# Kernel tuning notes

Measured on AMD Instinct MI355X. Metric: run time of the kernel, lower is better.

The kernel has to match this reference:

```python
import jax, jax.numpy as jnp
import numpy as np

M, N, K, C, G = 16384, 131072, 16, 128, 8
EPS_BN = 1e-5


def _bn(x, g, b):
    # inference-mode BatchNorm1d (running_mean=0, running_var=1)
    return x * (g / jnp.sqrt(1.0 + EPS_BN)) + b


def setup_inputs() -> dict:
    key = jax.random.key(0)
    ks = jax.random.split(key, 16)
    f32 = jnp.float32
    s = 0.05
    return {
        "query_feat": jax.random.normal(ks[0], (M, C), f32),
        "context_feat": jax.random.normal(ks[1], (N, C), f32),
        "query_coord": jax.random.normal(ks[2], (M, 3), f32),
        "context_coord": jax.random.normal(ks[3], (N, 3), f32),
        "Wq": jax.random.normal(ks[4], (C, C), f32) * s,
        "bq": jnp.zeros((C,), f32),
        "gq": jnp.ones((C,), f32),
        "betaq": jnp.zeros((C,), f32),
        "Wk": jax.random.normal(ks[5], (C, C), f32) * s,
        "bk": jnp.zeros((C,), f32),
        "gk": jnp.ones((C,), f32),
        "betak": jnp.zeros((C,), f32),
        "Wv": jax.random.normal(ks[6], (C, C), f32) * s,
        "bv": jnp.zeros((C,), f32),
        "Wp1": jax.random.normal(ks[7], (3, C), f32) * s,
        "bp1": jnp.zeros((C,), f32),
        "gp1": jnp.ones((C,), f32),
        "betap1": jnp.zeros((C,), f32),
        "Wp2": jax.random.normal(ks[8], (C, C), f32) * s,
        "bp2": jnp.zeros((C,), f32),
        "Ww1": jax.random.normal(ks[9], (C, G), f32) * s,
        "bw1": jnp.zeros((G,), f32),
        "gw1": jnp.ones((G,), f32),
        "betaw1": jnp.zeros((G,), f32),
        "Ww2": jax.random.normal(ks[10], (G, G), f32) * s,
        "bw2": jnp.zeros((G,), f32),
        "knn_indexes": jax.random.randint(ks[11], (M, K), 0, N, dtype=jnp.int32),
    }


def reference(query_feat, context_feat, query_coord, context_coord,
              Wq, bq, gq, betaq, Wk, bk, gk, betak, Wv, bv,
              Wp1, bp1, gp1, betap1, Wp2, bp2,
              Ww1, bw1, gw1, betaw1, Ww2, bw2, knn_indexes):
    q = jax.nn.relu(_bn(query_feat @ Wq + bq, gq, betaq))              # (M, C)
    k = jax.nn.relu(_bn(context_feat @ Wk + bk, gk, betak))            # (N, C)
    v = context_feat @ Wv + bv                                         # (N, C)

    mask = knn_indexes >= 0                                            # (M, K); -1 = padded neighbor
    idx = jnp.where(mask, knn_indexes, 0)
    mf = mask[..., None].astype(q.dtype)                               # (M, K, 1)

    key_g = k[idx] * mf                                                # (M, K, C) gather (zero row for -1)
    val_g = v[idx] * mf                                                # (M, K, C)
    pos = (context_coord[idx] - query_coord[:, None, :]) * mf          # (M, K, 3) relative position

    # positional-encoding bias branch (pe_bias=True, pe_multiplier=False)
    peb = jax.nn.relu(_bn(pos @ Wp1 + bp1, gp1, betap1)) @ Wp2 + bp2   # (M, K, C)
    rel = key_g - q[:, None, :] + peb                                  # (M, K, C)
    val_g = val_g + peb

    # grouped vector attention weights
    w = jax.nn.relu(_bn(rel @ Ww1 + bw1, gw1, betaw1)) @ Ww2 + bw2     # (M, K, G)
    w = jax.nn.softmax(w, axis=1) * mf                                 # softmax over neighbors, mask padded

    m_, k_ = idx.shape
    c_ = q.shape[-1]
    g_ = w.shape[-1]
    out = jnp.einsum('mkgi,mkg->mgi', val_g.reshape(m_, k_, g_, c_ // g_), w)
    return out.reshape(m_, c_)
```

## Files before the change

### kernel.cpp

```cpp
#include <hip/hip_runtime.h>

#define C 128
#define G 8
#define KNN 16
#define QB 4
#define EPS 1e-5f

typedef unsigned short u16;
typedef __attribute__((ext_vector_type(8))) short short8;
typedef __attribute__((ext_vector_type(4))) float float4v;

union frag_u { short8 v; u16 u[8]; };

__device__ inline u16 f2bf(float f) {
    unsigned u = __builtin_bit_cast(unsigned, f);
    unsigned r = (u + 0x7fffu + ((u >> 16) & 1u)) >> 16;
    return (u16)r;
}
__device__ inline float bf2f(u16 h) {
    unsigned u = ((unsigned)h) << 16;
    return __builtin_bit_cast(float, u);
}

__global__ __launch_bounds__(256) void prep_w(
    const float* __restrict__ Wk, const float* __restrict__ Wv,
    const float* __restrict__ Wq, const float* __restrict__ Wp2,
    const float* __restrict__ Ww1, u16* __restrict__ dst)
{
    const int b = blockIdx.x, t = threadIdx.x;
    if (b < 16) {
        const int mi = b >> 2, qt = b & 3;
        const float* W = mi == 0 ? Wk : mi == 1 ? Wv : mi == 2 ? Wq : Wp2;
        u16* d = dst + mi * 16384;
        for (int e = qt * 4096 + t; e < (qt + 1) * 4096; e += 256) {
            const int k = e >> 7, n = e & 127;
            const int cb = n >> 4, lan = n & 15;
            const int kk = k >> 5, quad = (k >> 3) & 3, j = k & 7;
            d[(((cb * 4 + kk) * 4 + quad) * 16 + lan) * 8 + j] = f2bf(W[e]);
        }
    } else {
        u16* d = dst + 4 * 16384;
        for (int e = t; e < 4096; e += 256) {
            const int j = e & 7, lan = (e >> 3) & 15;
            const int quad = (e >> 7) & 3, kk = e >> 9;
            const int k = kk * 32 + quad * 8 + j;
            d[e] = lan < 8 ? f2bf(Ww1[k * G + lan]) : (u16)0;
        }
    }
}

__global__ __launch_bounds__(256) void proj_all(
    const float* __restrict__ Xc, const float* __restrict__ Xq,
    const u16* __restrict__ PWk, const float* __restrict__ bk,
    const float* __restrict__ gk, const float* __restrict__ betak,
    const u16* __restrict__ PWv, const float* __restrict__ bv,
    const u16* __restrict__ PWq, const float* __restrict__ bq,
    const float* __restrict__ gq, const float* __restrict__ betaq,
    u16* __restrict__ kout, u16* __restrict__ vout, u16* __restrict__ qout,
    int nkv)
{
    __shared__ u16 Xs[64 * 136];
    const int t = threadIdx.x;
    const int w = t >> 6, l = t & 63;
    const int quad = l >> 4, lan = l & 15;
    const bool isq = (int)blockIdx.x >= nkv;
    const long long row0 = (long long)(isq ? blockIdx.x - nkv : blockIdx.x) * 64;
    const float* X = isq ? Xq : Xc;

    {
        const float4* Xv = (const float4*)(X + row0 * C);
#pragma unroll
        for (int i = 0; i < 8; i++) {
            const int e = t + 256 * i;
            const int r = e >> 5, c4 = e & 31;
            const float4 f = Xv[e];
            uint2 p;
            p.x = (unsigned)f2bf(f.x) | ((unsigned)f2bf(f.y) << 16);
            p.y = (unsigned)f2bf(f.z) | ((unsigned)f2bf(f.w) << 16);
            *(uint2*)(&Xs[r * 136 + c4 * 4]) = p;
        }
    }
    __syncthreads();

    if (!isq) {
        unsigned vp[2][4][2];
        {
            short8 Bf[2][4];
#pragma unroll
            for (int ct = 0; ct < 2; ct++) {
                const int cb = w * 2 + ct;
#pragma unroll
                for (int kk = 0; kk < 4; kk++)
                    Bf[ct][kk] = *(const short8*)(PWv + (((cb * 4 + kk) * 4 + quad) * 16 + lan) * 8);
            }
            float4v acc[2][4];
#pragma unroll
            for (int ct = 0; ct < 2; ct++)
#pragma unroll
                for (int rt = 0; rt < 4; rt++) acc[ct][rt] = (float4v)0.f;
#pragma unroll
            for (int rt = 0; rt < 4; rt++)
#pragma unroll
                for (int kk = 0; kk < 4; kk++) {
                    const short8 A = *(const short8*)(&Xs[(rt * 16 + lan) * 136 + kk * 32 + quad * 8]);
#pragma unroll
                    for (int ct = 0; ct < 2; ct++)
                        acc[ct][rt] = __builtin_amdgcn_mfma_f32_16x16x32_bf16(
                            A, Bf[ct][kk], acc[ct][rt], 0, 0, 0);
                }
#pragma unroll
            for (int ct = 0; ct < 2; ct++) {
                const float bb = bv[w * 32 + ct * 16 + lan];
#pragma unroll
                for (int rt = 0; rt < 4; rt++)
#pragma unroll
                    for (int h = 0; h < 2; h++)
                        vp[ct][rt][h] = (unsigned)f2bf(acc[ct][rt][2 * h] + bb)
                                      | ((unsigned)f2bf(acc[ct][rt][2 * h + 1] + bb) << 16);
            }
        }
        float4v acck[2][4];
        {
            short8 Bf[2][4];
#pragma unroll
            for (int ct = 0; ct < 2; ct++) {
                const int cb = w * 2 + ct;
#pragma unroll
                for (int kk = 0; kk < 4; kk++)
                    Bf[ct][kk] = *(const short8*)(PWk + (((cb * 4 + kk) * 4 + quad) * 16 + lan) * 8);
            }
#pragma unroll
            for (int ct = 0; ct < 2; ct++)
#pragma unroll
                for (int rt = 0; rt < 4; rt++) acck[ct][rt] = (float4v)0.f;
#pragma unroll
            for (int rt = 0; rt < 4; rt++)
#pragma unroll
                for (int kk = 0; kk < 4; kk++) {
                    const short8 A = *(const short8*)(&Xs[(rt * 16 + lan) * 136 + kk * 32 + quad * 8]);
#pragma unroll
                    for (int ct = 0; ct < 2; ct++)
                        acck[ct][rt] = __builtin_amdgcn_mfma_f32_16x16x32_bf16(
                            A, Bf[ct][kk], acck[ct][rt], 0, 0, 0);
                }
        }
        __syncthreads();

#pragma unroll
        for (int ct = 0; ct < 2; ct++) {
            const int cg = w * 32 + ct * 16 + lan;
            const float bb = bk[cg];
            const float sc = gk[cg] * rsqrtf(1.f + EPS);
            const float sh = betak[cg];
#pragma unroll
            for (int rt = 0; rt < 4; rt++)
#pragma unroll
                for (int reg = 0; reg < 4; reg++) {
                    float y = (acck[ct][rt][reg] + bb) * sc + sh;
                    y = y > 0.f ? y : 0.f;
                    Xs[(rt * 16 + quad * 4 + reg) * 136 + cg] = f2bf(y);
                }
        }
        __syncthreads();
#pragma unroll
        for (int i = 0; i < 4; i++) {
            const int e = t + 256 * i;
            const int r = e >> 4, cc = (e & 15) * 8;
            *(short8*)(kout + (row0 + r) * C + cc) = *(const short8*)(&Xs[r * 136 + cc]);
        }
        __syncthreads();

#pragma unroll
        for (int ct = 0; ct < 2; ct++) {
            const int cg = w * 32 + ct * 16 + lan;
#pragma unroll
            for (int rt = 0; rt < 4; rt++)
#pragma unroll
                for (int h = 0; h < 2; h++) {
                    Xs[(rt * 16 + quad * 4 + 2 * h) * 136 + cg]     = (u16)(vp[ct][rt][h] & 0xffffu);
                    Xs[(rt * 16 + quad * 4 + 2 * h + 1) * 136 + cg] = (u16)(vp[ct][rt][h] >> 16);
                }
        }
        __syncthreads();
#pragma unroll
        for (int i = 0; i < 4; i++) {
            const int e = t + 256 * i;
            const int r = e >> 4, cc = (e & 15) * 8;
            *(short8*)(vout + (row0 + r) * C + cc) = *(const short8*)(&Xs[r * 136 + cc]);
        }
    } else {
        short8 Bf[2][4];
#pragma unroll
        for (int ct = 0; ct < 2; ct++) {
            const int cb = w * 2 + ct;
#pragma unroll
            for (int kk = 0; kk < 4; kk++)
                Bf[ct][kk] = *(const short8*)(PWq + (((cb * 4 + kk) * 4 + quad) * 16 + lan) * 8);
        }
        float4v acc[2][4];
#pragma unroll
        for (int ct = 0; ct < 2; ct++)
#pragma unroll
            for (int rt = 0; rt < 4; rt++) acc[ct][rt] = (float4v)0.f;
#pragma unroll
        for (int rt = 0; rt < 4; rt++)
#pragma unroll
            for (int kk = 0; kk < 4; kk++) {
                const short8 A = *(const short8*)(&Xs[(rt * 16 + lan) * 136 + kk * 32 + quad * 8]);
#pragma unroll
                for (int ct = 0; ct < 2; ct++)
                    acc[ct][rt] = __builtin_amdgcn_mfma_f32_16x16x32_bf16(
                        A, Bf[ct][kk], acc[ct][rt], 0, 0, 0);
            }
        __syncthreads();
#pragma unroll
        for (int ct = 0; ct < 2; ct++) {
            const int cg = w * 32 + ct * 16 + lan;
            const float bb = bq[cg];
            const float sc = gq[cg] * rsqrtf(1.f + EPS);
            const float sh = betaq[cg];
#pragma unroll
            for (int rt = 0; rt < 4; rt++)
#pragma unroll
                for (int reg = 0; reg < 4; reg++) {
                    float y = (acc[ct][rt][reg] + bb) * sc + sh;
                    y = y > 0.f ? y : 0.f;
                    Xs[(rt * 16 + quad * 4 + reg) * 136 + cg] = f2bf(y);
                }
        }
        __syncthreads();
#pragma unroll
        for (int i = 0; i < 4; i++) {
            const int e = t + 256 * i;
            const int r = e >> 4, cc = (e & 15) * 8;
            *(short8*)(qout + (row0 + r) * C + cc) = *(const short8*)(&Xs[r * 136 + cc]);
        }
    }
}

__global__ __launch_bounds__(256) void attn5(
    const u16* __restrict__ qbuf, const u16* __restrict__ kbuf,
    const u16* __restrict__ vbuf,
    const float* __restrict__ qcoord, const float* __restrict__ ccoord,
    const float* __restrict__ Wp1, const float* __restrict__ bp1,
    const float* __restrict__ gp1, const float* __restrict__ betap1,
    const u16* __restrict__ PWp2, const float* __restrict__ bp2,
    const u16* __restrict__ PWw1, const float* __restrict__ bw1,
    const float* __restrict__ gw1, const float* __restrict__ betaw1,
    const float* __restrict__ Ww2, const float* __restrict__ bw2,
    const int* __restrict__ knn, float* __restrict__ out)
{
    __shared__ u16   fA[64 * 136];
    __shared__ float pxs[64], pys[64], pzs[64];
    __shared__ int   idxs[64];
    __shared__ float wl[QB * 16 * G];

    const int t = threadIdx.x;
    const int w = t >> 6, l = t & 63;
    const int quad = l >> 4, lan = l & 15;
    const int m0 = blockIdx.x * QB;
    const int rsub = t >> 4;
    const int c8 = (t & 15) * 8;

    if (t < 64) {
        const int q = t >> 4;
        const int ii = knn[(m0 + q) * KNN + (t & 15)];
        const float mf = ii >= 0 ? 1.f : 0.f;
        const int i0 = ii >= 0 ? ii : 0;
        idxs[t] = ii;
        pxs[t] = (ccoord[i0 * 3 + 0] - qcoord[(m0 + q) * 3 + 0]) * mf;
        pys[t] = (ccoord[i0 * 3 + 1] - qcoord[(m0 + q) * 3 + 1]) * mf;
        pzs[t] = (ccoord[i0 * 3 + 2] - qcoord[(m0 + q) * 3 + 2]) * mf;
    }
    __syncthreads();

    {
        const int c = t & 127, hh = t >> 7;
        const float w0 = Wp1[c], w1_ = Wp1[C + c], w2_ = Wp1[2 * C + c];
        const float sc = gp1[c] * rsqrtf(1.f + EPS);
        const float bb = bp1[c], sh = betap1[c];
#pragma unroll
        for (int r2 = 0; r2 < 32; r2++) {
            const int r = hh * 32 + r2;
            float y = fmaf(pxs[r], w0, fmaf(pys[r], w1_, fmaf(pzs[r], w2_, bb)));
            y = y * sc + sh;
            y = y > 0.f ? y : 0.f;
            fA[r * 136 + c] = f2bf(y);
        }
    }
    __syncthreads();

    float4v acc[2][4];
    {
        short8 Bf[2][4];
#pragma unroll
        for (int ct = 0; ct < 2; ct++) {
            const int cb = w * 2 + ct;
#pragma unroll
            for (int kk = 0; kk < 4; kk++)
                Bf[ct][kk] = *(const short8*)(PWp2 + (((cb * 4 + kk) * 4 + quad) * 16 + lan) * 8);
        }
#pragma unroll
        for (int ct = 0; ct < 2; ct++)
#pragma unroll
            for (int q = 0; q < 4; q++) acc[ct][q] = (float4v)0.f;
#pragma unroll
        for (int q = 0; q < 4; q++)
#pragma unroll
            for (int kk = 0; kk < 4; kk++) {
                const short8 A = *(const short8*)(&fA[(q * 16 + lan) * 136 + kk * 32 + quad * 8]);
#pragma unroll
                for (int ct = 0; ct < 2; ct++)
                    acc[ct][q] = __builtin_amdgcn_mfma_f32_16x16x32_bf16(
                        A, Bf[ct][kk], acc[ct][q], 0, 0, 0);
            }
    }
    __syncthreads();

    {
        const float bb0 = bp2[w * 32 + lan];
        const float bb1 = bp2[w * 32 + 16 + lan];
#pragma unroll
        for (int ct = 0; ct < 2; ct++)
#pragma unroll
            for (int q = 0; q < 4; q++)
#pragma unroll
                for (int reg = 0; reg < 4; reg++)
                    fA[(q * 16 + quad * 4 + reg) * 136 + w * 32 + ct * 16 + lan] =
                        f2bf(acc[ct][q][reg] + (ct ? bb1 : bb0));
    }
    __syncthreads();

    short8 valr[4];
    {
#pragma unroll
        for (int p = 0; p < 4; p++) {
            const int r = p * 16 + rsub;
            const int ii = idxs[r];
            const float mf = ii >= 0 ? 1.f : 0.f;
            const size_t i0 = ii >= 0 ? ii : 0;
            frag_u kgv, vgv, qgv, peb, relv, valv;
            kgv.v = *(const short8*)(kbuf + i0 * C + c8);
            vgv.v = *(const short8*)(vbuf + i0 * C + c8);
            qgv.v = *(const short8*)(qbuf + (size_t)(m0 + p) * C + c8);
            peb.v = *(const short8*)(&fA[r * 136 + c8]);
#pragma unroll
            for (int j = 0; j < 8; j++) {
                const float pe = bf2f(peb.u[j]);
                relv.u[j] = f2bf(fmaf(bf2f(kgv.u[j]), mf, pe - bf2f(qgv.u[j])));
                valv.u[j] = f2bf(fmaf(bf2f(vgv.u[j]), mf, pe));
            }
            *(short8*)(&fA[r * 136 + c8]) = relv.v;
            valr[p] = valv.v;
        }
    }
    __syncthreads();

    {
        short8 Bw[4];
#pragma unroll
        for (int kk = 0; kk < 4; kk++)
            Bw[kk] = *(const short8*)(PWw1 + ((kk * 4 + quad) * 16 + lan) * 8);
        float4v a4 = (float4v)0.f;
#pragma unroll
        for (int kk = 0; kk < 4; kk++) {
            const short8 A = *(const short8*)(&fA[(w * 16 + lan) * 136 + kk * 32 + quad * 8]);
            a4 = __builtin_amdgcn_mfma_f32_16x16x32_bf16(A, Bw[kk], a4, 0, 0, 0);
        }
        if (lan < G) {
            const int g = lan;
            const float sc = gw1[g] * rsqrtf(1.f + EPS);
            const float bb = bw1[g], sh = betaw1[g];
#pragma unroll
            for (int reg = 0; reg < 4; reg++) {
                const int j = quad * 4 + reg;
                float y = (a4[reg] + bb) * sc + sh;
                wl[w * 128 + j * 8 + g] = y > 0.f ? y : 0.f;
            }
        }
    }
    __syncthreads();

#pragma unroll
    for (int p = 0; p < 4; p++)
        *(short8*)(&fA[(p * 16 + rsub) * 136 + c8]) = valr[p];

    if (t < QB * G) {
        const int q = t >> 3, g2 = t & 7;
        float w2c[G];
#pragma unroll
        for (int g = 0; g < G; g++) w2c[g] = Ww2[g * G + g2];
        const float bb = bw2[g2];
        float lg[KNN], mx = -1e30f;
#pragma unroll
        for (int j = 0; j < KNN; j++) {
            float a = bb;
#pragma unroll
            for (int g = 0; g < G; g++) a = fmaf(wl[q * 128 + j * 8 + g], w2c[g], a);
            lg[j] = a;
            mx = fmaxf(mx, a);
        }
        float sum = 0.f;
#pragma unroll
        for (int j = 0; j < KNN; j++) { lg[j] = __expf(lg[j] - mx); sum += lg[j]; }
        const float inv = 1.f / sum;
#pragma unroll
        for (int j = 0; j < KNN; j++) {
            const float mf = idxs[q * 16 + j] >= 0 ? 1.f : 0.f;
            wl[q * 128 + j * 8 + g2] = lg[j] * inv * mf;
        }
    }
    __syncthreads();

#pragma unroll
    for (int i = 0; i < 2; i++) {
        const int e = t + 256 * i;
        const int q = e >> 7, c = e & 127, g = c >> 4;
        float a = 0.f;
#pragma unroll
        for (int j = 0; j < KNN; j++)
            a = fmaf(bf2f(fA[(q * 16 + j) * 136 + c]), wl[q * 128 + j * 8 + g], a);
        out[(size_t)(m0 + q) * C + c] = a;
    }
}

extern "C" void kernel_launch(void* const* d_in, const int* in_sizes, int n_in,
                              void* d_out, int out_size, void* d_ws, size_t ws_size,
                              hipStream_t stream)
{
    const float* query_feat    = (const float*)d_in[0];
    const float* context_feat  = (const float*)d_in[1];
    const float* query_coord   = (const float*)d_in[2];
    const float* context_coord = (const float*)d_in[3];
    const float* Wq    = (const float*)d_in[4];
    const float* bq    = (const float*)d_in[5];
    const float* gq    = (const float*)d_in[6];
    const float* betaq = (const float*)d_in[7];
    const float* Wk    = (const float*)d_in[8];
    const float* bk    = (const float*)d_in[9];
    const float* gk    = (const float*)d_in[10];
    const float* betak = (const float*)d_in[11];
    const float* Wv    = (const float*)d_in[12];
    const float* bv    = (const float*)d_in[13];
    const float* Wp1   = (const float*)d_in[14];
    const float* bp1   = (const float*)d_in[15];
    const float* gp1   = (const float*)d_in[16];
    const float* betap1= (const float*)d_in[17];
    const float* Wp2   = (const float*)d_in[18];
    const float* bp2   = (const float*)d_in[19];
    const float* Ww1   = (const float*)d_in[20];
    const float* bw1   = (const float*)d_in[21];
    const float* gw1   = (const float*)d_in[22];
    const float* betaw1= (const float*)d_in[23];
    const float* Ww2   = (const float*)d_in[24];
    const float* bw2   = (const float*)d_in[25];
    const int*   knn   = (const int*)d_in[26];

    const int M = in_sizes[0] / C;
    const int N = in_sizes[1] / C;

    u16* kb = (u16*)d_ws;
    u16* vb = kb + (size_t)N * C;
    u16* qb = vb + (size_t)N * C;
    u16* pw = qb + (size_t)M * C;
    u16* pWk  = pw;
    u16* pWv  = pw + 16384;
    u16* pWq  = pw + 2 * 16384;
    u16* pWp2 = pw + 3 * 16384;
    u16* pWw1 = pw + 4 * 16384;

    prep_w<<<17, 256, 0, stream>>>(Wk, Wv, Wq, Wp2, Ww1, pw);
    proj_all<<<N / 64 + M / 64, 256, 0, stream>>>(
        context_feat, query_feat,
        pWk, bk, gk, betak, pWv, bv,
        pWq, bq, gq, betaq,
        kb, vb, qb, N / 64);
    attn5<<<M / QB, 256, 0, stream>>>(qb, kb, vb, query_coord, context_coord,
                                      Wp1, bp1, gp1, betap1, pWp2, bp2,
                                      pWw1, bw1, gw1, betaw1, Ww2, bw2,
                                      knn, (float*)d_out);
}
```

Before: 225.5 us.

## Fold Ww1 projection into K/Q/PE precompute to shrink gathered key data

Uses linearity of rel @ Ww1 = k@Ww1 - q@Ww1 + peb@Ww1 to project k and q down to 8 groups inside the projection kernel, storing K and Q as N×8 and M×8 instead of full 128-wide rows. Wp2@Ww1 and bp2@Ww1 are precomputed so the attention kernel gets the PE contribution from one extra MFMA. This removes the 128-channel key and query gathers and their full-width writes, and the value gather is now issued at kernel start to overlap with the PE work. The cost is extra MFMA work in the projection kernel and different bf16 rounding points, since the products are rounded to bf16 at 8 channels.

```diff
diff --git a/kernel.cpp b/kernel.cpp
--- a/kernel.cpp
+++ b/kernel.cpp
@@ -25,7 +25,8 @@
 __global__ __launch_bounds__(256) void prep_w(
     const float* __restrict__ Wk, const float* __restrict__ Wv,
     const float* __restrict__ Wq, const float* __restrict__ Wp2,
-    const float* __restrict__ Ww1, u16* __restrict__ dst)
+    const float* __restrict__ Ww1, const float* __restrict__ bp2,
+    u16* __restrict__ dst, float* __restrict__ cw1)
 {
     const int b = blockIdx.x, t = threadIdx.x;
     if (b < 16) {
@@ -38,13 +39,31 @@
             const int kk = k >> 5, quad = (k >> 3) & 3, j = k & 7;
             d[(((cb * 4 + kk) * 4 + quad) * 16 + lan) * 8 + j] = f2bf(W[e]);
         }
-    } else {
+    } else if (b == 16) {
         u16* d = dst + 4 * 16384;
         for (int e = t; e < 4096; e += 256) {
             const int j = e & 7, lan = (e >> 3) & 15;
             const int quad = (e >> 7) & 3, kk = e >> 9;
             const int k = kk * 32 + quad * 8 + j;
             d[e] = lan < 8 ? f2bf(Ww1[k * G + lan]) : (u16)0;
+        }
+    } else {
+        u16* d = dst + 4 * 16384 + 4096;
+        for (int e = t; e < 4096; e += 256) d[e] = 0;
+        __syncthreads();
+#pragma unroll
+        for (int it = 0; it < 4; it++) {
+            const int k = it * 32 + (t >> 3), g = t & 7;
+            float a = 0.f;
+            for (int i = 0; i < C; i++)
+                a = fmaf(Wp2[k * C + i], Ww1[i * G + g], a);
+            const int kk = k >> 5, quad = (k >> 3) & 3, j = k & 7;
+            d[((kk * 4 + quad) * 16 + g) * 8 + j] = f2bf(a);
+        }
+        if (t < G) {
+            float a = 0.f;
+            for (int i = 0; i < C; i++) a = fmaf(bp2[i], Ww1[i * G + t], a);
+            cw1[t] = a;
         }
     }
 }
@@ -56,7 +75,8 @@
     const u16* __restrict__ PWv, const float* __restrict__ bv,
     const u16* __restrict__ PWq, const float* __restrict__ bq,
     const float* __restrict__ gq, const float* __restrict__ betaq,
-    u16* __restrict__ kout, u16* __restrict__ vout, u16* __restrict__ qout,
+    const u16* __restrict__ PWw1b,
+    u16* __restrict__ vout, u16* __restrict__ Kp, u16* __restrict__ Qp,
     int nkv)
 {
     __shared__ u16 Xs[64 * 136];
@@ -162,11 +182,23 @@
                 }
         }
         __syncthreads();
-#pragma unroll
-        for (int i = 0; i < 4; i++) {
-            const int e = t + 256 * i;
-            const int r = e >> 4, cc = (e & 15) * 8;
-            *(short8*)(kout + (row0 + r) * C + cc) = *(const short8*)(&Xs[r * 136 + cc]);
+
+        {
+            short8 Bw[4];
+#pragma unroll
+            for (int kk = 0; kk < 4; kk++)
+                Bw[kk] = *(const short8*)(PWw1b + ((kk * 4 + quad) * 16 + lan) * 8);
+            float4v ka = (float4v)0.f;
+#pragma unroll
+            for (int kk = 0; kk < 4; kk++) {
+                const short8 A = *(const short8*)(&Xs[(w * 16 + lan) * 136 + kk * 32 + quad * 8]);
+                ka = __builtin_amdgcn_mfma_f32_16x16x32_bf16(A, Bw[kk], ka, 0, 0, 0);
+            }
+            if (lan < G) {
+#pragma unroll
+                for (int reg = 0; reg < 4; reg++)
+                    Kp[(row0 + w * 16 + quad * 4 + reg) * G + lan] = f2bf(ka[reg]);
+            }
         }
         __syncthreads();
 
@@ -189,29 +221,31 @@
             *(short8*)(vout + (row0 + r) * C + cc) = *(const short8*)(&Xs[r * 136 + cc]);
         }
     } else {
-        short8 Bf[2][4];
-#pragma unroll
-        for (int ct = 0; ct < 2; ct++) {
-            const int cb = w * 2 + ct;
-#pragma unroll
-            for (int kk = 0; kk < 4; kk++)
-                Bf[ct][kk] = *(const short8*)(PWq + (((cb * 4 + kk) * 4 + quad) * 16 + lan) * 8);
-        }
         float4v acc[2][4];
-#pragma unroll
-        for (int ct = 0; ct < 2; ct++)
-#pragma unroll
-            for (int rt = 0; rt < 4; rt++) acc[ct][rt] = (float4v)0.f;
-#pragma unroll
-        for (int rt = 0; rt < 4; rt++)
-#pragma unroll
-            for (int kk = 0; kk < 4; kk++) {
-                const short8 A = *(const short8*)(&Xs[(rt * 16 + lan) * 136 + kk * 32 + quad * 8]);
-#pragma unroll
-                for (int ct = 0; ct < 2; ct++)
-                    acc[ct][rt] = __builtin_amdgcn_mfma_f32_16x16x32_bf16(
-                        A, Bf[ct][kk], acc[ct][rt], 0, 0, 0);
-            }
+        {
+            short8 Bf[2][4];
+#pragma unroll
+            for (int ct = 0; ct < 2; ct++) {
+                const int cb = w * 2 + ct;
+#pragma unroll
+                for (int kk = 0; kk < 4; kk++)
+                    Bf[ct][kk] = *(const short8*)(PWq + (((cb * 4 + kk) * 4 + quad) * 16 + lan) * 8);
+            }
+#pragma unroll
+            for (int ct = 0; ct < 2; ct++)
+#pragma unroll
+                for (int rt = 0; rt < 4; rt++) acc[ct][rt] = (float4v)0.f;
+#pragma unroll
+            for (int rt = 0; rt < 4; rt++)
+#pragma unroll
+                for (int kk = 0; kk < 4; kk++) {
+                    const short8 A = *(const short8*)(&Xs[(rt * 16 + lan) * 136 + kk * 32 + quad * 8]);
+#pragma unroll
+                    for (int ct = 0; ct < 2; ct++)
+                        acc[ct][rt] = __builtin_amdgcn_mfma_f32_16x16x32_bf16(
+                            A, Bf[ct][kk], acc[ct][rt], 0, 0, 0);
+                }
+        }
         __syncthreads();
 #pragma unroll
         for (int ct = 0; ct < 2; ct++) {
@@ -229,28 +263,44 @@
                 }
         }
         __syncthreads();
-#pragma unroll
-        for (int i = 0; i < 4; i++) {
-            const int e = t + 256 * i;
-            const int r = e >> 4, cc = (e & 15) * 8;
-            *(short8*)(qout + (row0 + r) * C + cc) = *(const short8*)(&Xs[r * 136 + cc]);
+        {
+            short8 Bw[4];
+#pragma unroll
+            for (int kk = 0; kk < 4; kk++)
+                Bw[kk] = *(const short8*)(PWw1b + ((kk * 4 + quad) * 16 + lan) * 8);
+            float4v qa = (float4v)0.f;
+#pragma unroll
+            for (int kk = 0; kk < 4; kk++) {
+                const short8 A = *(const short8*)(&Xs[(w * 16 + lan) * 136 + kk * 32 + quad * 8]);
+                qa = __builtin_amdgcn_mfma_f32_16x16x32_bf16(A, Bw[kk], qa, 0, 0, 0);
+            }
+            if (lan < G) {
+#pragma unroll
+                for (int reg = 0; reg < 4; reg++)
+                    Qp[(row0 + w * 16 + quad * 4 + reg) * G + lan] = f2bf(qa[reg]);
+            }
         }
     }
 }
 
-__global__ __launch_bounds__(256) void attn5(
-    const u16* __restrict__ qbuf, const u16* __restrict__ kbuf,
-    const u16* __restrict__ vbuf,
+__global__ __launch_bounds__(256) void attn6(
+    const u16* __restrict__ vbuf, const u16* __restrict__ Kp,
+    const u16* __restrict__ Qp,
     const float* __restrict__ qcoord, const float* __restrict__ ccoord,
     const float* __restrict__ Wp1, const float* __restrict__ bp1,
     const float* __restrict__ gp1, const float* __restrict__ betap1,
     const u16* __restrict__ PWp2, const float* __restrict__ bp2,
-    const u16* __restrict__ PWw1, const float* __restrict__ bw1,
+    const u16* __restrict__ PWp2pb, const float* __restrict__ cw1,
+    const float* __restrict__ bw1,
     const float* __restrict__ gw1, const float* __restrict__ betaw1,
     const float* __restrict__ Ww2, const float* __restrict__ bw2,
     const int* __restrict__ knn, float* __restrict__ out)
 {
     __shared__ u16   fA[64 * 136];
+    __shared__ u16   kgs[64 * G];
+    __shared__ float qps[QB * G];
+    __shared__ float pebp[64 * G];
+    __shared__ float cw1s[G];
     __shared__ float pxs[64], pys[64], pzs[64];
     __shared__ int   idxs[64];
     __shared__ float wl[QB * 16 * G];
@@ -262,15 +312,33 @@
     const int rsub = t >> 4;
     const int c8 = (t & 15) * 8;
 
+    float mfr[4];
+    frag_u vg[4];
+#pragma unroll
+    for (int p = 0; p < 4; p++) {
+        const int ii = knn[m0 * KNN + p * 16 + rsub];
+        mfr[p] = ii >= 0 ? 1.f : 0.f;
+        const size_t i0 = ii >= 0 ? ii : 0;
+        vg[p].v = *(const short8*)(vbuf + i0 * C + c8);
+    }
     if (t < 64) {
         const int q = t >> 4;
-        const int ii = knn[(m0 + q) * KNN + (t & 15)];
+        const int ii = knn[m0 * KNN + t];
         const float mf = ii >= 0 ? 1.f : 0.f;
         const int i0 = ii >= 0 ? ii : 0;
         idxs[t] = ii;
         pxs[t] = (ccoord[i0 * 3 + 0] - qcoord[(m0 + q) * 3 + 0]) * mf;
         pys[t] = (ccoord[i0 * 3 + 1] - qcoord[(m0 + q) * 3 + 1]) * mf;
         pzs[t] = (ccoord[i0 * 3 + 2] - qcoord[(m0 + q) * 3 + 2]) * mf;
+        *(short8*)(&kgs[t * G]) = *(const short8*)(Kp + (size_t)i0 * G);
+    } else if (t < 68) {
+        const int p = t - 64;
+        frag_u qv;
+        qv.v = *(const short8*)(Qp + (size_t)(m0 + p) * G);
+#pragma unroll
+        for (int j = 0; j < G; j++) qps[p * G + j] = bf2f(qv.u[j]);
+    } else if (t < 76) {
+        cw1s[t - 68] = cw1[t - 68];
     }
     __syncthreads();
 
@@ -291,6 +359,7 @@
     __syncthreads();
 
     float4v acc[2][4];
+    float4v pp = (float4v)0.f;
     {
         short8 Bf[2][4];
 #pragma unroll
@@ -314,6 +383,12 @@
                     acc[ct][q] = __builtin_amdgcn_mfma_f32_16x16x32_bf16(
                         A, Bf[ct][kk], acc[ct][q], 0, 0, 0);
             }
+#pragma unroll
+        for (int kk = 0; kk < 4; kk++) {
+            const short8 Bp = *(const short8*)(PWp2pb + ((kk * 4 + quad) * 16 + lan) * 8);
+            const short8 A = *(const short8*)(&fA[(w * 16 + lan) * 136 + kk * 32 + quad * 8]);
+            pp = __builtin_amdgcn_mfma_f32_16x16x32_bf16(A, Bp, pp, 0, 0, 0);
+        }
     }
     __syncthreads();
 
@@ -328,62 +403,39 @@
                 for (int reg = 0; reg < 4; reg++)
                     fA[(q * 16 + quad * 4 + reg) * 136 + w * 32 + ct * 16 + lan] =
                         f2bf(acc[ct][q][reg] + (ct ? bb1 : bb0));
-    }
-    __syncthreads();
-
-    short8 valr[4];
+        if (lan < G) {
+#pragma unroll
+            for (int reg = 0; reg < 4; reg++)
+                pebp[(w * 16 + quad * 4 + reg) * G + lan] = pp[reg];
+        }
+    }
+    __syncthreads();
+
     {
 #pragma unroll
         for (int p = 0; p < 4; p++) {
             const int r = p * 16 + rsub;
-            const int ii = idxs[r];
-            const float mf = ii >= 0 ? 1.f : 0.f;
-            const size_t i0 = ii >= 0 ? ii : 0;
-            frag_u kgv, vgv, qgv, peb, relv, valv;
-            kgv.v = *(const short8*)(kbuf + i0 * C + c8);
-            vgv.v = *(const short8*)(vbuf + i0 * C + c8);
-            qgv.v = *(const short8*)(qbuf + (size_t)(m0 + p) * C + c8);
+            const float mf = mfr[p];
+            frag_u peb, valv;
             peb.v = *(const short8*)(&fA[r * 136 + c8]);
 #pragma unroll
-            for (int j = 0; j < 8; j++) {
-                const float pe = bf2f(peb.u[j]);
-                relv.u[j] = f2bf(fmaf(bf2f(kgv.u[j]), mf, pe - bf2f(qgv.u[j])));
-                valv.u[j] = f2bf(fmaf(bf2f(vgv.u[j]), mf, pe));
-            }
-            *(short8*)(&fA[r * 136 + c8]) = relv.v;
-            valr[p] = valv.v;
-        }
-    }
-    __syncthreads();
-
-    {
-        short8 Bw[4];
-#pragma unroll
-        for (int kk = 0; kk < 4; kk++)
-            Bw[kk] = *(const short8*)(PWw1 + ((kk * 4 + quad) * 16 + lan) * 8);
-        float4v a4 = (float4v)0.f;
-#pragma unroll
-        for (int kk = 0; kk < 4; kk++) {
-            const short8 A = *(const short8*)(&fA[(w * 16 + lan) * 136 + kk * 32 + quad * 8]);
-            a4 = __builtin_amdgcn_mfma_f32_16x16x32_bf16(A, Bw[kk], a4, 0, 0, 0);
-        }
-        if (lan < G) {
-            const int g = lan;
-            const float sc = gw1[g] * rsqrtf(1.f + EPS);
-            const float bb = bw1[g], sh = betaw1[g];
-#pragma unroll
-            for (int reg = 0; reg < 4; reg++) {
-                const int j = quad * 4 + reg;
-                float y = (a4[reg] + bb) * sc + sh;
-                wl[w * 128 + j * 8 + g] = y > 0.f ? y : 0.f;
-            }
-        }
-    }
-    __syncthreads();
-
-#pragma unroll
-    for (int p = 0; p < 4; p++)
-        *(short8*)(&fA[(p * 16 + rsub) * 136 + c8]) = valr[p];
+            for (int j = 0; j < 8; j++)
+                valv.u[j] = f2bf(fmaf(bf2f(vg[p].u[j]), mf, bf2f(peb.u[j])));
+            *(short8*)(&fA[r * 136 + c8]) = valv.v;
+        }
+    }
+    if (t < 64) {
+        const int q = t >> 4, j = t & 15;
+        const float mf = idxs[t] >= 0 ? 1.f : 0.f;
+#pragma unroll
+        for (int g = 0; g < G; g++) {
+            const float L = bf2f(kgs[t * G + g]) * mf - qps[q * G + g]
+                          + pebp[t * G + g] + cw1s[g] + bw1[g];
+            const float y = L * (gw1[g] * rsqrtf(1.f + EPS)) + betaw1[g];
+            wl[q * 128 + j * G + g] = y > 0.f ? y : 0.f;
+        }
+    }
+    __syncthreads();
 
     if (t < QB * G) {
         const int q = t >> 3, g2 = t & 7;
@@ -459,24 +511,26 @@
     const int M = in_sizes[0] / C;
     const int N = in_sizes[1] / C;
 
-    u16* kb = (u16*)d_ws;
-    u16* vb = kb + (size_t)N * C;
-    u16* qb = vb + (size_t)N * C;
-    u16* pw = qb + (size_t)M * C;
-    u16* pWk  = pw;
-    u16* pWv  = pw + 16384;
-    u16* pWq  = pw + 2 * 16384;
-    u16* pWp2 = pw + 3 * 16384;
-    u16* pWw1 = pw + 4 * 16384;
-
-    prep_w<<<17, 256, 0, stream>>>(Wk, Wv, Wq, Wp2, Ww1, pw);
+    u16* vb = (u16*)d_ws;
+    u16* Kp = vb + (size_t)N * C;
+    u16* Qp = Kp + (size_t)N * G;
+    u16* pw = Qp + (size_t)M * G;
+    u16* pWk    = pw;
+    u16* pWv    = pw + 16384;
+    u16* pWq    = pw + 2 * 16384;
+    u16* pWp2   = pw + 3 * 16384;
+    u16* pWw1b  = pw + 4 * 16384;
+    u16* pWp2pb = pw + 4 * 16384 + 4096;
+    float* cw1  = (float*)(pw + 4 * 16384 + 2 * 4096);
+
+    prep_w<<<18, 256, 0, stream>>>(Wk, Wv, Wq, Wp2, Ww1, bp2, pw, cw1);
     proj_all<<<N / 64 + M / 64, 256, 0, stream>>>(
         context_feat, query_feat,
         pWk, bk, gk, betak, pWv, bv,
-        pWq, bq, gq, betaq,
-        kb, vb, qb, N / 64);
-    attn5<<<M / QB, 256, 0, stream>>>(qb, kb, vb, query_coord, context_coord,
+        pWq, bq, gq, betaq, pWw1b,
+        vb, Kp, Qp, N / 64);
+    attn6<<<M / QB, 256, 0, stream>>>(vb, Kp, Qp, query_coord, context_coord,
                                       Wp1, bp1, gp1, betap1, pWp2, bp2,
-                                      pWw1, bw1, gw1, betaw1, Ww2, bw2,
+                                      pWp2pb, cw1, bw1, gw1, betaw1, Ww2, bw2,
                                       knn, (float*)d_out);
 }
```

Measured after the change: 218.8 us. 1.03x faster.
